# Kernel tuning notes

Hardware: AMD Instinct MI355X
Metric: run time of the kernel (lower is better)

## Reference

```python
import jax, jax.numpy as jnp
import numpy as np

N_HEAD = 12


def setup_inputs() -> dict:
    key = jax.random.key(0)
    k1, k2, k3, k4 = jax.random.split(key, 4)
    B, T, C = 2, 2048, 768
    x = jax.random.normal(k1, (B, T, C), jnp.float32)
    eps = 0.1 * jnp.abs(jax.random.normal(k2, (B, T, C), jnp.float32))
    return {
        "x": x,
        "x_lower": x - eps,
        "x_upper": x + eps,
        "W_attn": 0.02 * jax.random.normal(k3, (3 * C, C), jnp.float32),
        "W_proj": 0.02 * jax.random.normal(k4, (C, C), jnp.float32),
    }


def _sdpa(q, k, v):
    # q,k,v: [B,H,T,D]; causal softmax attention
    T = q.shape[-2]
    scale = 1.0 / np.sqrt(q.shape[-1]).astype(np.float32)
    att = jnp.einsum('bhqd,bhkd->bhqk', q, k) * scale
    mask = jnp.tril(jnp.ones((T, T), dtype=bool))
    att = jnp.where(mask, att, -jnp.inf)
    att = jax.nn.softmax(att, axis=-1)
    return jnp.einsum('bhqk,bhkd->bhqd', att, v)


def reference(x, x_lower, x_upper, W_attn, W_proj):
    B, T, C = x.shape
    H = N_HEAD
    D = C // H

    def qkv(inp, W):
        out = inp @ W.T  # [B,T,3C]
        q, k, v = jnp.split(out, 3, axis=-1)
        hd = lambda t: t.reshape(B, T, H, D).transpose(0, 2, 1, 3)
        return hd(q), hd(k), hd(v)

    # nominal path
    q, k, v = qkv(x, W_attn)

    # signed weight split: positive keeps W>=0 entries, negative keeps W<0
    Wp = jnp.maximum(W_attn, 0.0)
    Wn = jnp.minimum(W_attn, 0.0)

    qup, kup, vup = qkv(x_upper, Wp)
    qun, kun, vun = qkv(x_upper, Wn)
    qlp, klp, vlp = qkv(x_lower, Wp)
    qln, kln, vln = qkv(x_lower, Wn)

    q_lo, q_hi = qlp + qun, qup + qln
    k_lo, k_hi = klp + kun, kup + kln
    v_lo, v_hi = vlp + vun, vup + vln

    y = _sdpa(q, k, v)
    # 8 interval-bound SDPA branches (q outer, k mid, v inner: lll..uuu)
    combos = [
        _sdpa(qa, ka, va)
        for qa in (q_lo, q_hi)
        for ka in (k_lo, k_hi)
        for va in (v_lo, v_hi)
    ]
    y_all = jnp.stack(combos, axis=0)  # [8,B,H,T,D]
    y_lo = y_all.min(axis=0)
    y_hi = y_all.max(axis=0)

    merge = lambda t: t.transpose(0, 2, 1, 3).reshape(B, T, C)
    return (merge(y) @ W_proj.T, merge(y_lo) @ W_proj.T, merge(y_hi) @ W_proj.T)
```

## Files before the change

kernel.cpp:

```cpp
#include <hip/hip_runtime.h>
#include <hip/hip_bf16.h>
#include <cstdint>

typedef float f4  __attribute__((ext_vector_type(4)));
typedef short s8v __attribute__((ext_vector_type(8)));
typedef int   i4v __attribute__((ext_vector_type(4)));

#define BHTD 3145728
#define BTC  3145728
#define NT   2048
#define NC   768
#define NWA  1769472
#define NWP  589824
#define NEG  -1e30f
#define QSCALE 0.18033688f

static __device__ __forceinline__ short bfbits(float f) {
    return __builtin_bit_cast(short, __float2bfloat16(f));
}
static __device__ __forceinline__ float bf2f(short s) {
    return __builtin_bit_cast(float, (int)(((unsigned int)(unsigned short)s) << 16));
}
static __device__ __forceinline__ float exp2fast(float x) {
    return __builtin_amdgcn_exp2f(x);
}
static __device__ __forceinline__ int cvtpk_bf16(float lo, float hi) {
    int r;
    asm("v_cvt_pk_bf16_f32 %0, %1, %2" : "=v"(r) : "v"(lo), "v"(hi));
    return r;
}
static __device__ __forceinline__ float rowred_max(float x) {
    x = fmaxf(x, __shfl_xor(x, 16, 64));
    x = fmaxf(x, __shfl_xor(x, 32, 64));
    return x;
}
static __device__ __forceinline__ float rowred_sum(float x) {
    x += __shfl_xor(x, 16, 64);
    x += __shfl_xor(x, 32, 64);
    return x;
}

__global__ __launch_bounds__(256) void prep_cvt(
    const float* __restrict__ x, const float* __restrict__ xl,
    const float* __restrict__ xu, const float* __restrict__ W,
    const float* __restrict__ Wp,
    short* __restrict__ xn, short* __restrict__ xm, short* __restrict__ xr,
    short* __restrict__ wb, short* __restrict__ wpb)
{
    const size_t flat = (size_t)blockIdx.x * 256 + threadIdx.x;
    const size_t i = flat * 8;
    {
        const f4 a0 = *(const f4*)&x[i],  a1 = *(const f4*)&x[i + 4];
        const f4 l0 = *(const f4*)&xl[i], l1 = *(const f4*)&xl[i + 4];
        const f4 u0 = *(const f4*)&xu[i], u1 = *(const f4*)&xu[i + 4];
        s8v vn, vm, vr;
#pragma unroll
        for (int j = 0; j < 4; j++) {
            vn[j]     = bfbits(a0[j]);                   vn[4 + j] = bfbits(a1[j]);
            vm[j]     = bfbits(0.5f * (l0[j] + u0[j]));  vm[4 + j] = bfbits(0.5f * (l1[j] + u1[j]));
            vr[j]     = bfbits(0.5f * (u0[j] - l0[j]));  vr[4 + j] = bfbits(0.5f * (u1[j] - l1[j]));
        }
        *(s8v*)&xn[i] = vn;
        *(s8v*)&xm[i] = vm;
        *(s8v*)&xr[i] = vr;
    }
    if (flat < NWA / 8) {
        const size_t wi = flat * 8;
        const f4 w0 = *(const f4*)&W[wi], w1 = *(const f4*)&W[wi + 4];
        s8v vw;
#pragma unroll
        for (int j = 0; j < 4; j++) { vw[j] = bfbits(w0[j]); vw[4 + j] = bfbits(w1[j]); }
        *(s8v*)&wb[wi] = vw;
    }
    if (flat < NWP / 8) {
        const size_t wi = flat * 8;
        const f4 w0 = *(const f4*)&Wp[wi], w1 = *(const f4*)&Wp[wi + 4];
        s8v vw;
#pragma unroll
        for (int j = 0; j < 4; j++) { vw[j] = bfbits(w0[j]); vw[4 + j] = bfbits(w1[j]); }
        *(s8v*)&wpb[wi] = vw;
    }
}

__global__ __launch_bounds__(256, 3) void qkv_proj_mfma(
    const short* __restrict__ xn, const short* __restrict__ xm,
    const short* __restrict__ xr, const short* __restrict__ wb,
    short* __restrict__ qkvb)
{
    __shared__ short sm[2][12800];
    short* Eb = &sm[0][0];

    const int b_  = blockIdx.x;
    const int xcd = b_ & 7;
    const int s_  = b_ >> 3;
    const int jx  = s_ % 18;
    const int ny  = xcd + 8 * (s_ / 18);
    const int j0 = jx * 128;
    const int n0 = ny * 64;
    const int t  = threadIdx.x;
    const int wv = t >> 6, lane = t & 63, quad = lane >> 4, l16 = lane & 15;
    const int rw = t >> 2, koff = (t & 3) * 8;

    f4 aN[8], aM[8], aR[8];
#pragma unroll
    for (int i = 0; i < 8; i++) { aN[i] = f4{0,0,0,0}; aM[i] = f4{0,0,0,0}; aR[i] = f4{0,0,0,0}; }

    const size_t abase  = (size_t)(n0 + rw) * NC + koff;
    const size_t bbase0 = (size_t)(j0 + rw) * NC + koff;
    const size_t bbase1 = (size_t)(j0 + 64 + rw) * NC + koff;

    s8v rn, rm, rr, rb0, rb1;
    rn  = *(const s8v*)&xn[abase];
    rm  = *(const s8v*)&xm[abase];
    rr  = *(const s8v*)&xr[abase];
    rb0 = *(const s8v*)&wb[bbase0];
    rb1 = *(const s8v*)&wb[bbase1];
    *(s8v*)&sm[0][rw * 40 + koff]               = rn;
    *(s8v*)&sm[0][2560 + rw * 40 + koff]        = rm;
    *(s8v*)&sm[0][5120 + rw * 40 + koff]        = rr;
    *(s8v*)&sm[0][7680 + rw * 40 + koff]        = rb0;
    *(s8v*)&sm[0][7680 + (rw + 64) * 40 + koff] = rb1;

    for (int it = 0; it < NC / 32; ++it) {
        const int cb = it & 1, nb = cb ^ 1;
        __syncthreads();
        const bool pf = (it + 1 < NC / 32);
        if (pf) {
            const size_t k1 = (size_t)(it + 1) * 32;
            rn  = *(const s8v*)&xn[abase + k1];
            rm  = *(const s8v*)&xm[abase + k1];
            rr  = *(const s8v*)&xr[abase + k1];
            rb0 = *(const s8v*)&wb[bbase0 + k1];
            rb1 = *(const s8v*)&wb[bbase1 + k1];
        }
        const s8v fx = *(const s8v*)&sm[cb][(wv * 16 + l16) * 40 + quad * 8];
        const s8v fm = *(const s8v*)&sm[cb][2560 + (wv * 16 + l16) * 40 + quad * 8];
        const s8v fr = *(const s8v*)&sm[cb][5120 + (wv * 16 + l16) * 40 + quad * 8];
#pragma unroll
        for (int nt = 0; nt < 8; ++nt) {
            const s8v fb = *(const s8v*)&sm[cb][7680 + (nt * 16 + l16) * 40 + quad * 8];
            i4v bi = __builtin_bit_cast(i4v, fb);
#pragma unroll
            for (int i = 0; i < 4; i++) bi[i] &= 0x7fff7fff;
            const s8v fa = __builtin_bit_cast(s8v, bi);
            aN[nt] = __builtin_amdgcn_mfma_f32_16x16x32_bf16(fx, fb, aN[nt], 0, 0, 0);
            aM[nt] = __builtin_amdgcn_mfma_f32_16x16x32_bf16(fm, fb, aM[nt], 0, 0, 0);
            aR[nt] = __builtin_amdgcn_mfma_f32_16x16x32_bf16(fr, fa, aR[nt], 0, 0, 0);
        }
        if (pf) {
            *(s8v*)&sm[nb][rw * 40 + koff]               = rn;
            *(s8v*)&sm[nb][2560 + rw * 40 + koff]        = rm;
            *(s8v*)&sm[nb][5120 + rw * 40 + koff]        = rr;
            *(s8v*)&sm[nb][7680 + rw * 40 + koff]        = rb0;
            *(s8v*)&sm[nb][7680 + (rw + 64) * 40 + koff] = rb1;
        }
    }

    const int p = j0 / NC, hh0 = (j0 % NC) >> 6;
    const float osc = (p == 0) ? QSCALE : 1.0f;
    const int cc16 = (t & 3) * 16;
    for (int var = 0; var < 3; ++var)
        for (int h2 = 0; h2 < 2; ++h2) {
            __syncthreads();
#pragma unroll
            for (int nt4 = 0; nt4 < 4; ++nt4) {
                const int nt = h2 * 4 + nt4;
#pragma unroll
                for (int r = 0; r < 4; ++r) {
                    const float v = (var == 0) ? aN[nt][r]
                                  : (var == 1) ? aM[nt][r] - aR[nt][r]
                                               : aM[nt][r] + aR[nt][r];
                    Eb[(wv * 16 + quad * 4 + r) * 72 + nt4 * 16 + l16] = bfbits(v * osc);
                }
            }
            __syncthreads();
            const int hh = hh0 + h2;
            short* dst = qkvb + (size_t)(var * 3 + p) * BHTD;
            if (p < 2) {
                const int token = n0 + rw, b = token >> 11, tt = token & 2047;
                const size_t o = ((size_t)(b * 12 + hh) * NT + tt) * 64 + cc16;
                *(s8v*)&dst[o]     = *(const s8v*)&Eb[rw * 72 + cc16];
                *(s8v*)&dst[o + 8] = *(const s8v*)&Eb[rw * 72 + cc16 + 8];
            } else {
                const int d = rw;
                s8v e0, e1;
#pragma unroll
                for (int i = 0; i < 8; i++) e0[i] = Eb[(cc16 + i) * 72 + d];
#pragma unroll
                for (int i = 0; i < 8; i++) e1[i] = Eb[(cc16 + 8 + i) * 72 + d];
                const int token0 = n0 + cc16, b = token0 >> 11, tt = token0 & 2047;
                const size_t o = ((size_t)(b * 12 + hh) * 64 + d) * NT + tt;
                *(s8v*)&dst[o]     = e0;
                *(s8v*)&dst[o + 8] = e1;
            }
        }
}

__global__ __launch_bounds__(256) void flash_mfma(
    const short* __restrict__ qkvb, short* __restrict__ ybf,
    short* __restrict__ cand)
{
    const int b_  = blockIdx.x;
    const int xcd = b_ & 7;
    const int r_  = b_ >> 3;
    const int pr  = r_ & 7;
    const int r2  = r_ >> 3;
    const int z   = r2 % 5;
    const int bh  = xcd + 8 * (r2 / 5);
    const int t   = threadIdx.x;
    const int wv = t >> 6, lane = t & 63, quad = lane >> 4, l16 = lane & 15;
    const bool TWO = (z != 0);

    __shared__ short Ks[2][32 * 70];
    __shared__ short Vs[2][2][64 * 40];

    int sv, qvi, kvi, v0i, v1i;
    if (TWO) { sv = z; qvi = (sv + 1) >> 1; kvi = 2 - (sv & 1); v0i = 1; v1i = 2; }
    else     { sv = 0; qvi = 0; kvi = 0; v0i = 0; v1i = 0; }

    const size_t hb = (size_t)bh * (NT * 64);
    const short* Qp  = qkvb + (size_t)(qvi * 3 + 0) * BHTD + hb;
    const short* Kp  = qkvb + (size_t)(kvi * 3 + 1) * BHTD + hb;
    const short* V0p = qkvb + (size_t)(v0i * 3 + 2) * BHTD + hb;
    const short* V1p = qkvb + (size_t)(v1i * 3 + 2) * BHTD + hb;

    const int skr = t >> 3, skc = (t & 7) * 8;
    const int svd = t >> 2, svc = (t & 3) * 8;
    const int sig = (l16 >> 2) * 8 + (l16 & 3);

    for (int half = 0; half < 2; ++half) {
        const int qt = half ? (15 - pr) : pr;
        const int q0 = qt * 128;

        s8v qf[2][2];
#pragma unroll
        for (int mt = 0; mt < 2; ++mt)
#pragma unroll
            for (int ch = 0; ch < 2; ++ch)
                qf[mt][ch] = *(const s8v*)&Qp[(size_t)(q0 + 32 * wv + 16 * mt + l16) * 64 + ch * 32 + quad * 8];

        float mi[2], li[2];
        mi[0] = mi[1] = NEG; li[0] = li[1] = 0.f;
        f4 acc0[2][4], acc1[2][4];
#pragma unroll
        for (int mt = 0; mt < 2; ++mt)
#pragma unroll
            for (int i = 0; i < 4; ++i) { acc0[mt][i] = f4{0,0,0,0}; acc1[mt][i] = f4{0,0,0,0}; }

        const int ktn  = 4 * qt + 4;
        const int mykt = 4 * qt + wv + 1;

        __syncthreads();
        s8v rK, rV0, rV1;
        rK  = *(const s8v*)&Kp[(size_t)skr * 64 + skc];
        rV0 = *(const s8v*)&V0p[(size_t)svd * NT + svc];
        if (TWO) rV1 = *(const s8v*)&V1p[(size_t)svd * NT + svc];
        *(s8v*)&Ks[0][skr * 70 + skc]    = rK;
        *(s8v*)&Vs[0][0][svd * 40 + svc] = rV0;
        if (TWO) *(s8v*)&Vs[0][1][svd * 40 + svc] = rV1;

        for (int kt = 0; kt < ktn; ++kt) {
            const int k0 = kt * 32;
            const int cb = kt & 1, nb = cb ^ 1;
            __syncthreads();
            const bool pf = (kt + 1 < ktn);
            if (pf) {
                const int k1 = k0 + 32;
                rK  = *(const s8v*)&Kp[(size_t)(k1 + skr) * 64 + skc];
                rV0 = *(const s8v*)&V0p[(size_t)svd * NT + k1 + svc];
                if (TWO) rV1 = *(const s8v*)&V1p[(size_t)svd * NT + k1 + svc];
            }
            if (kt < mykt) {
                f4 s[2][2];
#pragma unroll
                for (int mt = 0; mt < 2; ++mt) { s[mt][0] = f4{0,0,0,0}; s[mt][1] = f4{0,0,0,0}; }
                __builtin_amdgcn_s_setprio(1);
#pragma unroll
                for (int nt = 0; nt < 2; ++nt)
#pragma unroll
                    for (int ch = 0; ch < 2; ++ch) {
                        const s8v kf = *(const s8v*)&Ks[cb][(sig + nt * 4) * 70 + ch * 32 + quad * 8];
                        s[0][nt] = __builtin_amdgcn_mfma_f32_16x16x32_bf16(kf, qf[0][ch], s[0][nt], 0, 0, 0);
                        s[1][nt] = __builtin_amdgcn_mfma_f32_16x16x32_bf16(kf, qf[1][ch], s[1][nt], 0, 0, 0);
                    }
                __builtin_amdgcn_s_setprio(0);

                s8v pa[2];
#pragma unroll
                for (int mt = 0; mt < 2; ++mt) {
                    const int rowb = q0 + 32 * wv + 16 * mt;
                    const int qrow = rowb + l16;
                    float a[8];
#pragma unroll
                    for (int nt = 0; nt < 2; ++nt)
#pragma unroll
                        for (int r = 0; r < 4; ++r) a[nt * 4 + r] = s[mt][nt][r];
                    if (k0 + 31 > rowb) {
#pragma unroll
                        for (int nt = 0; nt < 2; ++nt)
#pragma unroll
                            for (int r = 0; r < 4; ++r)
                                if (k0 + quad * 8 + nt * 4 + r > qrow) a[nt * 4 + r] = NEG;
                    }
                    const float c = fmaxf(fmaxf(fmaxf(a[0], a[1]), fmaxf(a[2], a[3])),
                                          fmaxf(fmaxf(a[4], a[5]), fmaxf(a[6], a[7])));
                    if (__any(c - mi[mt] > 8.0f)) {
                        const float mx = rowred_max(c);
                        const float nm = fmaxf(mi[mt], mx);
                        const float al = exp2fast(mi[mt] - nm);
                        mi[mt] = nm;
                        li[mt] *= al;
#pragma unroll
                        for (int r = 0; r < 4; ++r) {
                            const float alr = __shfl(al, (lane & 48) | (quad * 4 + r), 64);
#pragma unroll
                            for (int dt = 0; dt < 4; ++dt) acc0[mt][dt][r] *= alr;
                            if (TWO) {
#pragma unroll
                                for (int dt = 0; dt < 4; ++dt) acc1[mt][dt][r] *= alr;
                            }
                        }
                    }
                    float p[8];
#pragma unroll
                    for (int j = 0; j < 8; ++j) p[j] = exp2fast(a[j] - mi[mt]);
                    li[mt] += ((p[0] + p[1]) + (p[2] + p[3])) + ((p[4] + p[5]) + (p[6] + p[7]));
                    i4v pi;
#pragma unroll
                    for (int jj = 0; jj < 4; ++jj)
                        pi[jj] = cvtpk_bf16(p[2 * jj], p[2 * jj + 1]);
                    pa[mt] = __builtin_bit_cast(s8v, pi);
                }
                __builtin_amdgcn_s_setprio(1);
#pragma unroll
                for (int dt = 0; dt < 4; ++dt) {
                    const s8v vf0 = *(const s8v*)&Vs[cb][0][(dt * 16 + l16) * 40 + quad * 8];
                    acc0[0][dt] = __builtin_amdgcn_mfma_f32_16x16x32_bf16(pa[0], vf0, acc0[0][dt], 0, 0, 0);
                    acc0[1][dt] = __builtin_amdgcn_mfma_f32_16x16x32_bf16(pa[1], vf0, acc0[1][dt], 0, 0, 0);
                    if (TWO) {
                        const s8v vf1 = *(const s8v*)&Vs[cb][1][(dt * 16 + l16) * 40 + quad * 8];
                        acc1[0][dt] = __builtin_amdgcn_mfma_f32_16x16x32_bf16(pa[0], vf1, acc1[0][dt], 0, 0, 0);
                        acc1[1][dt] = __builtin_amdgcn_mfma_f32_16x16x32_bf16(pa[1], vf1, acc1[1][dt], 0, 0, 0);
                    }
                }
                __builtin_amdgcn_s_setprio(0);
            }
            if (pf) {
                *(s8v*)&Ks[nb][skr * 70 + skc]    = rK;
                *(s8v*)&Vs[nb][0][svd * 40 + svc] = rV0;
                if (TWO) *(s8v*)&Vs[nb][1][svd * 40 + svc] = rV1;
            }
        }

#pragma unroll
        for (int mt = 0; mt < 2; ++mt) {
            const float invq = 1.f / rowred_sum(li[mt]);
            float inv[4];
#pragma unroll
            for (int r = 0; r < 4; ++r)
                inv[r] = __shfl(invq, (lane & 48) | (quad * 4 + r), 64);
#pragma unroll
            for (int dt = 0; dt < 4; ++dt)
#pragma unroll
                for (int r = 0; r < 4; ++r) {
                    const size_t o = hb + (size_t)(q0 + 32 * wv + 16 * mt + quad * 4 + r) * 64 + dt * 16 + l16;
                    if (!TWO) {
                        ybf[o] = bfbits(acc0[mt][dt][r] * inv[r]);
                    } else {
                        const float xa = acc0[mt][dt][r] * inv[r];
                        const float xb = acc1[mt][dt][r] * inv[r];
                        cand[(size_t)(sv - 1) * BHTD + o] = bfbits(fminf(xa, xb));
                        cand[(size_t)(3 + sv) * BHTD + o] = bfbits(fmaxf(xa, xb));
                    }
                }
        }
    }
}

__global__ __launch_bounds__(256) void prep_out(short* __restrict__ cand)
{
    const size_t i = ((size_t)blockIdx.x * 256 + threadIdx.x) * 8;
    {
        const s8v c0 = *(const s8v*)&cand[i];
        const s8v c1 = *(const s8v*)&cand[(size_t)1 * BHTD + i];
        const s8v c2 = *(const s8v*)&cand[(size_t)2 * BHTD + i];
        const s8v c3 = *(const s8v*)&cand[(size_t)3 * BHTD + i];
        s8v lo;
#pragma unroll
        for (int j = 0; j < 8; j++) {
            const float v = fminf(fminf(bf2f(c0[j]), bf2f(c1[j])),
                                  fminf(bf2f(c2[j]), bf2f(c3[j])));
            lo[j] = (short)(__builtin_bit_cast(unsigned int, v) >> 16);
        }
        *(s8v*)&cand[i] = lo;
    }
    {
        const s8v c0 = *(const s8v*)&cand[(size_t)4 * BHTD + i];
        const s8v c1 = *(const s8v*)&cand[(size_t)5 * BHTD + i];
        const s8v c2 = *(const s8v*)&cand[(size_t)6 * BHTD + i];
        const s8v c3 = *(const s8v*)&cand[(size_t)7 * BHTD + i];
        s8v hi;
#pragma unroll
        for (int j = 0; j < 8; j++) {
            const float v = fmaxf(fmaxf(bf2f(c0[j]), bf2f(c1[j])),
                                  fmaxf(bf2f(c2[j]), bf2f(c3[j])));
            hi[j] = (short)(__builtin_bit_cast(unsigned int, v) >> 16);
        }
        *(s8v*)&cand[(size_t)4 * BHTD + i] = hi;
    }
}

__global__ __launch_bounds__(256) void out_proj_mfma(
    const short* __restrict__ ybf, const short* __restrict__ cand,
    const short* __restrict__ wpb, float* __restrict__ out)
{
    __shared__ short sm3[2][7680];
    float* Eb = (float*)sm3;

    const int b_  = blockIdx.x;
    const int xcd = b_ & 7;
    const int s_  = b_ >> 3;
    const int o   = s_ % 3;
    const int jx  = (s_ / 3) % 6;
    const int ny  = xcd + 8 * (s_ / 18);
    const int j0 = jx * 128, n0 = ny * 64;
    const int t  = threadIdx.x;
    const int wv = t >> 6, lane = t & 63, quad = lane >> 4, l16 = lane & 15;
    const int rw = t >> 2, koff = (t & 3) * 8;

    f4 acc[8];
#pragma unroll
    for (int i = 0; i < 8; i++) acc[i] = f4{0,0,0,0};

    const int token = n0 + rw, b = token >> 11, tt = token & 2047;
    const size_t wbase0 = (size_t)(j0 + rw) * NC + koff;
    const size_t wbase1 = (size_t)(j0 + 64 + rw) * NC + koff;
    const short* Ap = (o == 0) ? ybf : (o == 1) ? cand : cand + (size_t)4 * BHTD;

    s8v ra, rb0, rb1;
    auto loadTile = [&](int k1) {
        const int hh = k1 >> 6, d0 = (k1 & 63) + koff;
        const size_t aoff = ((size_t)(b * 12 + hh) * NT + tt) * 64 + d0;
        ra  = *(const s8v*)&Ap[aoff];
        rb0 = *(const s8v*)&wpb[wbase0 + k1];
        rb1 = *(const s8v*)&wpb[wbase1 + k1];
    };

    loadTile(0);
    *(s8v*)&sm3[0][rw * 40 + koff]               = ra;
    *(s8v*)&sm3[0][2560 + rw * 40 + koff]        = rb0;
    *(s8v*)&sm3[0][2560 + (rw + 64) * 40 + koff] = rb1;

    for (int it = 0; it < NC / 32; ++it) {
        const int cbuf = it & 1, nbuf = cbuf ^ 1;
        __syncthreads();
        const bool pf = (it + 1 < NC / 32);
        if (pf) loadTile((it + 1) * 32);
        const s8v af = *(const s8v*)&sm3[cbuf][(wv * 16 + l16) * 40 + quad * 8];
#pragma unroll
        for (int nt = 0; nt < 8; ++nt) {
            const s8v bf = *(const s8v*)&sm3[cbuf][2560 + (nt * 16 + l16) * 40 + quad * 8];
            acc[nt] = __builtin_amdgcn_mfma_f32_16x16x32_bf16(af, bf, acc[nt], 0, 0, 0);
        }
        if (pf) {
            *(s8v*)&sm3[nbuf][rw * 40 + koff]               = ra;
            *(s8v*)&sm3[nbuf][2560 + rw * 40 + koff]        = rb0;
            *(s8v*)&sm3[nbuf][2560 + (rw + 64) * 40 + koff] = rb1;
        }
    }
    const int cc = (t & 3) * 16;
    for (int h2 = 0; h2 < 2; ++h2) {
        __syncthreads();
#pragma unroll
        for (int nt4 = 0; nt4 < 4; ++nt4)
#pragma unroll
            for (int r = 0; r < 4; ++r)
                Eb[(wv * 16 + quad * 4 + r) * 68 + nt4 * 16 + l16] = acc[h2 * 4 + nt4][r];
        __syncthreads();
#pragma unroll
        for (int i = 0; i < 4; ++i) {
            const f4 vo = *(const f4*)&Eb[rw * 68 + cc + 4 * i];
            *(f4*)&out[(size_t)o * BTC + (size_t)(n0 + rw) * NC + j0 + h2 * 64 + cc + 4 * i] = vo;
        }
    }
}

extern "C" void kernel_launch(void* const* d_in, const int* in_sizes, int n_in,
                              void* d_out, int out_size, void* d_ws, size_t ws_size,
                              hipStream_t stream)
{
    const float* x  = (const float*)d_in[0];
    const float* xl = (const float*)d_in[1];
    const float* xu = (const float*)d_in[2];
    const float* Wa = (const float*)d_in[3];
    const float* Wp = (const float*)d_in[4];
    float* out = (float*)d_out;

    short* qkvb = (short*)d_ws;
    short* ybf  = qkvb + (size_t)9 * BHTD;
    short* cand = ybf + (size_t)BHTD;
    short* wpb  = cand + (size_t)8 * BHTD;

    short* xn = cand;
    short* xm = cand + (size_t)1 * BHTD;
    short* xr = cand + (size_t)2 * BHTD;
    short* wb = cand + (size_t)3 * BHTD;

    prep_cvt     <<<dim3(1536), 256, 0, stream>>>(x, xl, xu, Wa, Wp, xn, xm, xr, wb, wpb);
    qkv_proj_mfma<<<dim3(1152), 256, 0, stream>>>(xn, xm, xr, wb, qkvb);
    flash_mfma   <<<dim3(960),  256, 0, stream>>>(qkvb, ybf, cand);
    prep_out     <<<dim3(1536), 256, 0, stream>>>(cand);
    out_proj_mfma<<<dim3(1152), 256, 0, stream>>>(ybf, cand, wpb, out);
}
```

Baseline: 377.6 us.

## Use direct global-to-LDS loads with XOR swizzle in projection GEMMs

Both the QKV projection and output projection kernels now stage their bf16 tiles with global_load_lds DMA instead of loading into registers and writing to shared memory. The padded row layout is replaced by an unpadded 32-element stride with an XOR swizzle on the 16-byte chunk index, which shrinks the LDS footprint. The intent is to cut VGPR pressure and the LDS store instructions in the prefetch path. It relies on the barrier waiting for the async LDS writes to complete, and correctness depends on the swizzle matching between writer and reader.

```diff
diff --git a/kernel.cpp b/kernel.cpp
--- a/kernel.cpp
+++ b/kernel.cpp
@@ -28,6 +28,11 @@
     int r;
     asm("v_cvt_pk_bf16_f32 %0, %1, %2" : "=v"(r) : "v"(lo), "v"(hi));
     return r;
+}
+static __device__ __forceinline__ void gl_lds16(const short* g, short* l) {
+    __builtin_amdgcn_global_load_lds(
+        (const __attribute__((address_space(1))) void*)g,
+        (__attribute__((address_space(3))) void*)l, 16, 0, 0);
 }
 static __device__ __forceinline__ float rowred_max(float x) {
     x = fmaxf(x, __shfl_xor(x, 16, 64));
@@ -87,7 +92,7 @@
     const short* __restrict__ xr, const short* __restrict__ wb,
     short* __restrict__ qkvb)
 {
-    __shared__ short sm[2][12800];
+    __shared__ short sm[2][10240];
     short* Eb = &sm[0][0];
 
     const int b_  = blockIdx.x;
@@ -99,46 +104,46 @@
     const int n0 = ny * 64;
     const int t  = threadIdx.x;
     const int wv = t >> 6, lane = t & 63, quad = lane >> 4, l16 = lane & 15;
-    const int rw = t >> 2, koff = (t & 3) * 8;
+
+    const int srow = lane >> 2;
+    const int cswz = (lane & 3) ^ (srow & 3);
+
+    const size_t aoff  = (size_t)(n0 + wv * 16 + srow) * NC + cswz * 8;
+    const size_t boff0 = (size_t)(j0 + wv * 16 + srow) * NC + cswz * 8;
+    const size_t boff1 = (size_t)(j0 + 64 + wv * 16 + srow) * NC + cswz * 8;
+    const int lws = wv * 512;
 
     f4 aN[8], aM[8], aR[8];
 #pragma unroll
     for (int i = 0; i < 8; i++) { aN[i] = f4{0,0,0,0}; aM[i] = f4{0,0,0,0}; aR[i] = f4{0,0,0,0}; }
 
-    const size_t abase  = (size_t)(n0 + rw) * NC + koff;
-    const size_t bbase0 = (size_t)(j0 + rw) * NC + koff;
-    const size_t bbase1 = (size_t)(j0 + 64 + rw) * NC + koff;
-
-    s8v rn, rm, rr, rb0, rb1;
-    rn  = *(const s8v*)&xn[abase];
-    rm  = *(const s8v*)&xm[abase];
-    rr  = *(const s8v*)&xr[abase];
-    rb0 = *(const s8v*)&wb[bbase0];
-    rb1 = *(const s8v*)&wb[bbase1];
-    *(s8v*)&sm[0][rw * 40 + koff]               = rn;
-    *(s8v*)&sm[0][2560 + rw * 40 + koff]        = rm;
-    *(s8v*)&sm[0][5120 + rw * 40 + koff]        = rr;
-    *(s8v*)&sm[0][7680 + rw * 40 + koff]        = rb0;
-    *(s8v*)&sm[0][7680 + (rw + 64) * 40 + koff] = rb1;
+    {
+        gl_lds16(&xn[aoff],  &sm[0][0    + lws]);
+        gl_lds16(&xm[aoff],  &sm[0][2048 + lws]);
+        gl_lds16(&xr[aoff],  &sm[0][4096 + lws]);
+        gl_lds16(&wb[boff0], &sm[0][6144 + lws]);
+        gl_lds16(&wb[boff1], &sm[0][8192 + lws]);
+    }
+
+    const int rsw = (quad ^ (l16 & 3)) * 8;
 
     for (int it = 0; it < NC / 32; ++it) {
         const int cb = it & 1, nb = cb ^ 1;
         __syncthreads();
-        const bool pf = (it + 1 < NC / 32);
-        if (pf) {
+        if (it + 1 < NC / 32) {
             const size_t k1 = (size_t)(it + 1) * 32;
-            rn  = *(const s8v*)&xn[abase + k1];
-            rm  = *(const s8v*)&xm[abase + k1];
-            rr  = *(const s8v*)&xr[abase + k1];
-            rb0 = *(const s8v*)&wb[bbase0 + k1];
-            rb1 = *(const s8v*)&wb[bbase1 + k1];
-        }
-        const s8v fx = *(const s8v*)&sm[cb][(wv * 16 + l16) * 40 + quad * 8];
-        const s8v fm = *(const s8v*)&sm[cb][2560 + (wv * 16 + l16) * 40 + quad * 8];
-        const s8v fr = *(const s8v*)&sm[cb][5120 + (wv * 16 + l16) * 40 + quad * 8];
+            gl_lds16(&xn[aoff + k1],  &sm[nb][0    + lws]);
+            gl_lds16(&xm[aoff + k1],  &sm[nb][2048 + lws]);
+            gl_lds16(&xr[aoff + k1],  &sm[nb][4096 + lws]);
+            gl_lds16(&wb[boff0 + k1], &sm[nb][6144 + lws]);
+            gl_lds16(&wb[boff1 + k1], &sm[nb][8192 + lws]);
+        }
+        const s8v fx = *(const s8v*)&sm[cb][       (wv * 16 + l16) * 32 + rsw];
+        const s8v fm = *(const s8v*)&sm[cb][2048 + (wv * 16 + l16) * 32 + rsw];
+        const s8v fr = *(const s8v*)&sm[cb][4096 + (wv * 16 + l16) * 32 + rsw];
 #pragma unroll
         for (int nt = 0; nt < 8; ++nt) {
-            const s8v fb = *(const s8v*)&sm[cb][7680 + (nt * 16 + l16) * 40 + quad * 8];
+            const s8v fb = *(const s8v*)&sm[cb][6144 + (nt * 16 + l16) * 32 + rsw];
             i4v bi = __builtin_bit_cast(i4v, fb);
 #pragma unroll
             for (int i = 0; i < 4; i++) bi[i] &= 0x7fff7fff;
@@ -147,18 +152,11 @@
             aM[nt] = __builtin_amdgcn_mfma_f32_16x16x32_bf16(fm, fb, aM[nt], 0, 0, 0);
             aR[nt] = __builtin_amdgcn_mfma_f32_16x16x32_bf16(fr, fa, aR[nt], 0, 0, 0);
         }
-        if (pf) {
-            *(s8v*)&sm[nb][rw * 40 + koff]               = rn;
-            *(s8v*)&sm[nb][2560 + rw * 40 + koff]        = rm;
-            *(s8v*)&sm[nb][5120 + rw * 40 + koff]        = rr;
-            *(s8v*)&sm[nb][7680 + rw * 40 + koff]        = rb0;
-            *(s8v*)&sm[nb][7680 + (rw + 64) * 40 + koff] = rb1;
-        }
     }
 
     const int p = j0 / NC, hh0 = (j0 % NC) >> 6;
     const float osc = (p == 0) ? QSCALE : 1.0f;
-    const int cc16 = (t & 3) * 16;
+    const int rw = t >> 2, cc16 = (t & 3) * 16;
     for (int var = 0; var < 3; ++var)
         for (int h2 = 0; h2 < 2; ++h2) {
             __syncthreads();
@@ -414,7 +412,7 @@
     const short* __restrict__ ybf, const short* __restrict__ cand,
     const short* __restrict__ wpb, float* __restrict__ out)
 {
-    __shared__ short sm3[2][7680];
+    __shared__ short sm3[2][6144];
     float* Eb = (float*)sm3;
 
     const int b_  = blockIdx.x;
@@ -426,49 +424,49 @@
     const int j0 = jx * 128, n0 = ny * 64;
     const int t  = threadIdx.x;
     const int wv = t >> 6, lane = t & 63, quad = lane >> 4, l16 = lane & 15;
-    const int rw = t >> 2, koff = (t & 3) * 8;
+
+    const int srow = lane >> 2;
+    const int cswz = (lane & 3) ^ (srow & 3);
 
     f4 acc[8];
 #pragma unroll
     for (int i = 0; i < 8; i++) acc[i] = f4{0,0,0,0};
 
-    const int token = n0 + rw, b = token >> 11, tt = token & 2047;
-    const size_t wbase0 = (size_t)(j0 + rw) * NC + koff;
-    const size_t wbase1 = (size_t)(j0 + 64 + rw) * NC + koff;
+    const int tokenS = n0 + wv * 16 + srow;
+    const int bS = tokenS >> 11, ttS = tokenS & 2047;
+    const size_t abase = ((size_t)(bS * 12) * NT + ttS) * 64 + cswz * 8;
+    const size_t woff0 = (size_t)(j0 + wv * 16 + srow) * NC + cswz * 8;
+    const size_t woff1 = (size_t)(j0 + 64 + wv * 16 + srow) * NC + cswz * 8;
+    const int lws = wv * 512;
     const short* Ap = (o == 0) ? ybf : (o == 1) ? cand : cand + (size_t)4 * BHTD;
 
-    s8v ra, rb0, rb1;
-    auto loadTile = [&](int k1) {
-        const int hh = k1 >> 6, d0 = (k1 & 63) + koff;
-        const size_t aoff = ((size_t)(b * 12 + hh) * NT + tt) * 64 + d0;
-        ra  = *(const s8v*)&Ap[aoff];
-        rb0 = *(const s8v*)&wpb[wbase0 + k1];
-        rb1 = *(const s8v*)&wpb[wbase1 + k1];
-    };
-
-    loadTile(0);
-    *(s8v*)&sm3[0][rw * 40 + koff]               = ra;
-    *(s8v*)&sm3[0][2560 + rw * 40 + koff]        = rb0;
-    *(s8v*)&sm3[0][2560 + (rw + 64) * 40 + koff] = rb1;
+    {
+        gl_lds16(&Ap[abase],   &sm3[0][0    + lws]);
+        gl_lds16(&wpb[woff0],  &sm3[0][2048 + lws]);
+        gl_lds16(&wpb[woff1],  &sm3[0][4096 + lws]);
+    }
+
+    const int rsw = (quad ^ (l16 & 3)) * 8;
 
     for (int it = 0; it < NC / 32; ++it) {
         const int cbuf = it & 1, nbuf = cbuf ^ 1;
         __syncthreads();
-        const bool pf = (it + 1 < NC / 32);
-        if (pf) loadTile((it + 1) * 32);
-        const s8v af = *(const s8v*)&sm3[cbuf][(wv * 16 + l16) * 40 + quad * 8];
+        if (it + 1 < NC / 32) {
+            const int k1 = (it + 1) * 32;
+            const int hh = k1 >> 6, d0 = k1 & 63;
+            gl_lds16(&Ap[abase + (size_t)hh * (NT * 64) + d0], &sm3[nbuf][0    + lws]);
+            gl_lds16(&wpb[woff0 + k1],                         &sm3[nbuf][2048 + lws]);
+            gl_lds16(&wpb[woff1 + k1],                         &sm3[nbuf][4096 + lws]);
+        }
+        const s8v af = *(const s8v*)&sm3[cbuf][(wv * 16 + l16) * 32 + rsw];
 #pragma unroll
         for (int nt = 0; nt < 8; ++nt) {
-            const s8v bf = *(const s8v*)&sm3[cbuf][2560 + (nt * 16 + l16) * 40 + quad * 8];
+            const s8v bf = *(const s8v*)&sm3[cbuf][2048 + (nt * 16 + l16) * 32 + rsw];
             acc[nt] = __builtin_amdgcn_mfma_f32_16x16x32_bf16(af, bf, acc[nt], 0, 0, 0);
         }
-        if (pf) {
-            *(s8v*)&sm3[nbuf][rw * 40 + koff]               = ra;
-            *(s8v*)&sm3[nbuf][2560 + rw * 40 + koff]        = rb0;
-            *(s8v*)&sm3[nbuf][2560 + (rw + 64) * 40 + koff] = rb1;
-        }
-    }
-    const int cc = (t & 3) * 16;
+    }
+    const int rw = t >> 2, cc = (t & 3) * 16;
+    const int token = n0 + rw;
     for (int h2 = 0; h2 < 2; ++h2) {
         __syncthreads();
 #pragma unroll
@@ -480,7 +478,7 @@
 #pragma unroll
         for (int i = 0; i < 4; ++i) {
             const f4 vo = *(const f4*)&Eb[rw * 68 + cc + 4 * i];
-            *(f4*)&out[(size_t)o * BTC + (size_t)(n0 + rw) * NC + j0 + h2 * 64 + cc + 4 * i] = vo;
+            *(f4*)&out[(size_t)o * BTC + (size_t)token * NC + j0 + h2 * 64 + cc + 4 * i] = vo;
         }
     }
 }
```

Result: no change. 373.7 us (-1.0%).
